# Performance work log

Measured on AMD Instinct MI355X. Metric: run time of the kernel, lower is better.

## Reference

```python
import jax, jax.numpy as jnp
import numpy as np

N, E, C = 100000, 50000, 256
M, D, F, T = 128, 128, 128, 64
MSG = 2 * D + F + T  # 448
T_MAX = 100000


def setup_inputs() -> dict:
    key = jax.random.key(0)
    ks = jax.random.split(key, 16)
    src = jax.random.randint(ks[0], (E,), 0, N, dtype=jnp.int32)
    dst = jax.random.randint(ks[1], (E,), 0, N, dtype=jnp.int32)
    t = jnp.sort(jax.random.randint(ks[2], (E,), 0, T_MAX, dtype=jnp.int32))
    last_update = jax.random.randint(ks[3], (N,), 0, 1000, dtype=jnp.int32)
    event_feat = jax.random.normal(ks[4], (E, F), dtype=jnp.float32)
    src_embeds = jax.random.normal(ks[5], (E, D), dtype=jnp.float32)
    dst_embeds = jax.random.normal(ks[6], (E, D), dtype=jnp.float32)
    nodes_memory = jax.random.normal(ks[7], (N, M), dtype=jnp.float32)
    incidence = jax.random.uniform(ks[8], (N, C), dtype=jnp.float32)
    w_time = jax.random.normal(ks[9], (T,), dtype=jnp.float32)
    b_time = jax.random.normal(ks[10], (T,), dtype=jnp.float32)
    W_ih = jax.random.normal(ks[11], (MSG, 3 * M), dtype=jnp.float32) * 0.05
    W_hh = jax.random.normal(ks[12], (M, 3 * M), dtype=jnp.float32) * 0.05
    b_ih = jnp.zeros((3 * M,), jnp.float32)
    b_hh = jnp.zeros((3 * M,), jnp.float32)
    return dict(src=src, dst=dst, t=t, last_update=last_update,
                event_feat=event_feat, src_embeds=src_embeds, dst_embeds=dst_embeds,
                nodes_memory=nodes_memory, incidence=incidence,
                w_time=w_time, b_time=b_time, W_ih=W_ih, W_hh=W_hh,
                b_ih=b_ih, b_hh=b_hh)


def reference(src, dst, t, last_update, event_feat, src_embeds, dst_embeds,
              nodes_memory, incidence, w_time, b_time, W_ih, W_hh, b_ih, b_hh):
    E2 = 2 * E
    # store_events: raw messages + flipped-direction messages, keyed by source node
    src_all = jnp.concatenate([src, dst])            # [2E]
    emb_s = jnp.concatenate([src_embeds, dst_embeds], axis=0)
    emb_d = jnp.concatenate([dst_embeds, src_embeds], axis=0)
    feat = jnp.concatenate([event_feat, event_feat], axis=0)
    t_all = jnp.concatenate([t, t])                  # [2E]
    # message function: concat(src_embed, dst_embed, event_feat, time_encoding(dt))
    dt = (t_all - last_update[src_all]).astype(jnp.float32)
    time_enc = jnp.cos(dt[:, None] * w_time[None, :] + b_time[None, :])  # [2E, T]
    msg = jnp.concatenate([emb_s, emb_d, feat, time_enc], axis=-1)       # [2E, MSG]
    # 'last' aggregation: per-node argmax over timestamps via rank-encoded segment_max
    perm = jnp.argsort(t_all)  # ascending time order
    rank = jnp.zeros((E2,), jnp.int32).at[perm].set(jnp.arange(E2, dtype=jnp.int32))
    seg_rank = jax.ops.segment_max(rank, src_all, num_segments=N)
    counts = jax.ops.segment_sum(jnp.ones((E2,), jnp.int32), src_all, num_segments=N)
    has_msg = counts > 0                              # [N]
    last_idx = perm[jnp.where(has_msg, seg_rank, 0)]  # [N] event index of last message
    agg_msg = msg[last_idx]                           # [N, MSG]
    # GRU memory updater (torch.nn.GRUCell convention)
    gx = agg_msg @ W_ih + b_ih
    gh = nodes_memory @ W_hh + b_hh
    xr, xz, xn = jnp.split(gx, 3, axis=-1)
    hr, hz, hn = jnp.split(gh, 3, axis=-1)
    r = jax.nn.sigmoid(xr + hr)
    z = jax.nn.sigmoid(xz + hz)
    n = jnp.tanh(xn + r * hn)
    h_new = (1.0 - z) * n + z * nodes_memory
    new_mem = jnp.where(has_msg[:, None], h_new, nodes_memory)  # [N, M]
    # rewire_graph: community memory = incidence.T @ nodes_memory
    comm_mem = jnp.einsum('nc,nm->cm', incidence, new_mem)      # [C, M]
    return jnp.concatenate([new_mem, comm_mem], axis=0)         # [N + C, M]
```

## Files before the change

kernel.cpp:

```cpp
#include <hip/hip_runtime.h>
#include <hip/hip_bf16.h>
#include <stdint.h>

#define N_NODES   100000
#define N_EVENTS  50000
#define N_COMM    256
#define DIM_M     128
#define K_TOT     576
#define GCOLS     512
#define INV2PI    0.15915494309189535f

typedef float f32x4 __attribute__((ext_vector_type(4)));
typedef short s16x8 __attribute__((ext_vector_type(8)));
typedef short s16x4 __attribute__((ext_vector_type(4)));

#define KEYS_OFF   0
#define CNT_OFF    800000
#define LIST_OFF   800008
#define W2PI_OFF   1200128
#define B2PI_OFF   1200384
#define WT_OFF     1200640
#define X_ROWS     100096
#define X_OFF      1790464
#define PART_M_OFF X_OFF
#define CT_NCH     256
#define CT_CPN     392
#define TMP2_OFF   (PART_M_OFF + 33554432)
#define TENC_OFF   1790464
#define PART_F_OFF 14594560

__device__ inline unsigned short f2bf(float x) {
    union { float f; unsigned u; } v; v.f = x;
    unsigned r = v.u + 0x7FFFu + ((v.u >> 16) & 1u);
    return (unsigned short)(r >> 16);
}
__device__ inline float bf2f(unsigned short u) {
    union { unsigned u; float f; } v; v.u = ((unsigned)u) << 16;
    return v.f;
}
__device__ inline float cos_rev(float rev) {
    float fr = rev - floorf(rev);
#if __has_builtin(__builtin_amdgcn_cosf)
    return __builtin_amdgcn_cosf(fr);
#else
    return cosf(fr * 6.283185307179586f);
#endif
}
__device__ inline float sigmoid_f(float x) { return 1.0f / (1.0f + __expf(-x)); }
__device__ inline float tanh_f(float x) {
    float t = __expf(2.0f * x);
    return 1.0f - 2.0f / (t + 1.0f);
}

__global__ __launch_bounds__(256) void k_agg(const int* __restrict__ src,
                                             const int* __restrict__ dst,
                                             const int* __restrict__ t,
                                             unsigned long long* __restrict__ keys) {
    int i = blockIdx.x * 256 + threadIdx.x;
    if (i >= 2 * N_EVENTS) return;
    int e = (i < N_EVENTS) ? i : i - N_EVENTS;
    int node = (i < N_EVENTS) ? src[i] : dst[e];
    unsigned long long key =
        ((unsigned long long)(unsigned)t[e] << 32) | (unsigned)(i + 1);
    atomicMax(&keys[node], key);
}

__global__ __launch_bounds__(256) void k_compact(const unsigned long long* __restrict__ keys,
                                                 unsigned int* __restrict__ cnt,
                                                 int* __restrict__ list) {
    int n = blockIdx.x * 256 + threadIdx.x;
    if (n >= N_NODES) return;
    if (keys[n] != 0ULL) {
        unsigned p = atomicAdd(cnt, 1u);
        list[p] = n;
    }
}

__global__ void k_prep(const float* __restrict__ w_time, const float* __restrict__ b_time,
                       float* __restrict__ w2, float* __restrict__ b2) {
    int i = threadIdx.x;
    if (i < 64) { w2[i] = w_time[i] * INV2PI; b2[i] = b_time[i] * INV2PI; }
}

__global__ __launch_bounds__(256) void k_wconv(const float* __restrict__ W_ih,
                                               const float* __restrict__ W_hh,
                                               unsigned short* __restrict__ Wt) {
    int idx = blockIdx.x * 256 + threadIdx.x;
    if (idx >= GCOLS * K_TOT) return;
    int col2 = idx / K_TOT, k = idx % K_TOT;
    int mh = col2 >> 8, rem = col2 & 255;
    int g = rem >> 6, m = mh * 64 + (rem & 63);
    float v;
    if (g == 0)      v = (k < 448) ? W_ih[(size_t)k * 384 + m]
                                   : W_hh[(size_t)(k - 448) * 384 + m];
    else if (g == 1) v = (k < 448) ? W_ih[(size_t)k * 384 + 128 + m]
                                   : W_hh[(size_t)(k - 448) * 384 + 128 + m];
    else if (g == 2) v = (k < 448) ? W_ih[(size_t)k * 384 + 256 + m] : 0.0f;
    else             v = (k < 448) ? 0.0f : W_hh[(size_t)(k - 448) * 384 + 256 + m];
    Wt[idx] = f2bf(v);
}

__global__ __launch_bounds__(256) void k_wconv_old(const float* __restrict__ W_ih,
                                                   const float* __restrict__ W_hh,
                                                   unsigned short* __restrict__ Wt) {
    int idx = blockIdx.x * 256 + threadIdx.x;
    if (idx >= GCOLS * K_TOT) return;
    int col = idx / K_TOT, k = idx % K_TOT;
    float v;
    if (col < 256) {
        v = (k < 448) ? W_ih[(size_t)k * 384 + col]
                      : W_hh[(size_t)(k - 448) * 384 + col];
    } else if (col < 384) {
        v = (k < 448) ? W_ih[(size_t)k * 384 + col] : 0.0f;
    } else {
        v = (k < 448) ? 0.0f : W_hh[(size_t)(k - 448) * 384 + (col - 128)];
    }
    Wt[idx] = f2bf(v);
}

__global__ __launch_bounds__(256) void k_xbuild(
    const unsigned long long* __restrict__ keys,
    const unsigned int* __restrict__ cnt,
    const int* __restrict__ list,
    const int* __restrict__ t,
    const int* __restrict__ last_update,
    const float* __restrict__ event_feat,
    const float* __restrict__ src_embeds,
    const float* __restrict__ dst_embeds,
    const float* __restrict__ mem,
    const float* __restrict__ w2pi,
    const float* __restrict__ b2pi,
    unsigned short* __restrict__ X) {
    const unsigned c = *cnt;
    const unsigned cpad = (c + 127u) & ~127u;
    const unsigned total = cpad * 72u;
    for (unsigned idx = blockIdx.x * 256 + threadIdx.x; idx < total;
         idx += gridDim.x * 256) {
        const unsigned row = idx / 72u;
        const int s = (int)(idx - row * 72u);
        unsigned short* xp = X + (size_t)row * K_TOT + s * 8;
        s16x8 v;
        if (row >= c) {
#pragma unroll
            for (int j = 0; j < 8; ++j) v[j] = 0;
            *(s16x8*)xp = v;
            continue;
        }
        const int node = list[row];
        const unsigned long long key = keys[node];
        const int ia = (int)(key & 0xffffffffull) - 1;
        const int e = (ia < N_EVENTS) ? ia : ia - N_EVENTS;
        if (s < 48) {
            const float* p;
            if (s < 16)
                p = ((ia < N_EVENTS) ? src_embeds : dst_embeds) + (size_t)e * 128 + s * 8;
            else if (s < 32)
                p = ((ia < N_EVENTS) ? dst_embeds : src_embeds) + (size_t)e * 128 + (s - 16) * 8;
            else
                p = event_feat + (size_t)e * 128 + (s - 32) * 8;
            float4 a = *(const float4*)p;
            float4 b = *(const float4*)(p + 4);
            v[0] = (short)f2bf(a.x); v[1] = (short)f2bf(a.y);
            v[2] = (short)f2bf(a.z); v[3] = (short)f2bf(a.w);
            v[4] = (short)f2bf(b.x); v[5] = (short)f2bf(b.y);
            v[6] = (short)f2bf(b.z); v[7] = (short)f2bf(b.w);
        } else if (s < 56) {
            const float dt = (float)(t[e] - last_update[node]);
            const int c0 = (s - 48) * 8;
#pragma unroll
            for (int j = 0; j < 8; ++j) {
                float rev = fmaf(dt, w2pi[c0 + j], b2pi[c0 + j]);
                v[j] = (short)f2bf(cos_rev(rev));
            }
        } else {
            const float* p = mem + (size_t)node * 128 + (s - 56) * 8;
            float4 a = *(const float4*)p;
            float4 b = *(const float4*)(p + 4);
            v[0] = (short)f2bf(a.x); v[1] = (short)f2bf(a.y);
            v[2] = (short)f2bf(a.z); v[3] = (short)f2bf(a.w);
            v[4] = (short)f2bf(b.x); v[5] = (short)f2bf(b.y);
            v[6] = (short)f2bf(b.z); v[7] = (short)f2bf(b.w);
        }
        *(s16x8*)xp = v;
    }
}

__global__ __launch_bounds__(512, 4) void k_gemm2(
    const unsigned int* __restrict__ cnt,
    const int* __restrict__ list,
    const unsigned short* __restrict__ X,
    const unsigned short* __restrict__ Wt,
    const float* __restrict__ b_ih,
    const float* __restrict__ b_hh,
    float* __restrict__ out) {
    __shared__ unsigned short As[3][128][64];
    __shared__ unsigned short Bs[3][256][64];
    __shared__ int Ls[128];

    const unsigned c = *cnt;
    const int rb = blockIdx.x >> 1;
    const int mh = blockIdx.x & 1;
    const int base = rb * 128;
    if ((unsigned)base >= c) return;
    const int tid = threadIdx.x;
    const int w = tid >> 6, l = tid & 63;
    const int lr = l & 15, lk = l >> 4;
    const int wm = w >> 2, wn = w & 3;

    if (tid < 128)
        Ls[tid] = ((unsigned)(base + tid) < c) ? list[base + tid] : 0;

    const int r8 = tid >> 3;
    const int sj = tid & 7;
    const int srcsl = (sj ^ (r8 & 7)) << 3;
    const unsigned short* gA0 = X + (size_t)(base + r8) * K_TOT + srcsl;
    const unsigned short* gA1 = X + (size_t)(base + 64 + r8) * K_TOT + srcsl;
    const unsigned short* gB0 = Wt + (size_t)(mh * 256 + r8) * K_TOT + srcsl;

#define GLD(SRC, DST) __builtin_amdgcn_global_load_lds( \
        (const __attribute__((address_space(1))) unsigned int*)(SRC), \
        (__attribute__((address_space(3))) unsigned int*)(DST), 16, 0, 0)

    auto stage = [&](int ch, int buf) {
        GLD(gA0 + ch * 64, &As[buf][w * 8][0]);
        GLD(gA1 + ch * 64, &As[buf][64 + w * 8][0]);
        GLD(gB0 + ch * 64,                          &Bs[buf][w * 8][0]);
        GLD(gB0 + (size_t)64 * K_TOT + ch * 64,     &Bs[buf][64 + w * 8][0]);
        GLD(gB0 + (size_t)128 * K_TOT + ch * 64,    &Bs[buf][128 + w * 8][0]);
        GLD(gB0 + (size_t)192 * K_TOT + ch * 64,    &Bs[buf][192 + w * 8][0]);
    };

    f32x4 acc[4][4];
#pragma unroll
    for (int rt = 0; rt < 4; ++rt)
#pragma unroll
        for (int i = 0; i < 4; ++i) acc[rt][i] = (f32x4){0.f, 0.f, 0.f, 0.f};

    stage(0, 0);
    stage(1, 1);
    __syncthreads();

#pragma unroll
    for (int ch = 0; ch < 9; ++ch) {
        const int buf = ch % 3;
        if (ch <= 6) stage(ch + 2, (ch + 2) % 3);
        __builtin_amdgcn_s_setprio(1);
#pragma unroll
        for (int ks = 0; ks < 2; ++ks) {
            s16x8 a[4];
#pragma unroll
            for (int rt = 0; rt < 4; ++rt) {
                const int r = wm * 64 + rt * 16 + lr;
                const int sl = (ks * 4 + lk) ^ (r & 7);
                a[rt] = *(const s16x8*)&As[buf][r][sl << 3];
            }
#pragma unroll
            for (int i = 0; i < 4; ++i) {
                const int col = i * 64 + wn * 16 + lr;
                const int slb = (ks * 4 + lk) ^ (col & 7);
                s16x8 b = *(const s16x8*)&Bs[buf][col][slb << 3];
#pragma unroll
                for (int rt = 0; rt < 4; ++rt)
                    acc[rt][i] = __builtin_amdgcn_mfma_f32_16x16x32_bf16(
                        a[rt], b, acc[rt][i], 0, 0, 0);
            }
        }
        __builtin_amdgcn_s_setprio(0);
        if (ch < 8) {
            __builtin_amdgcn_sched_barrier(0);
            if (ch < 7) asm volatile("s_waitcnt vmcnt(6)" ::: "memory");
            else        asm volatile("s_waitcnt vmcnt(0)" ::: "memory");
            __builtin_amdgcn_s_barrier();
            __builtin_amdgcn_sched_barrier(0);
        }
    }

    const int mcol = mh * 64 + wn * 16 + lr;
    const float b_r  = b_ih[mcol] + b_hh[mcol];
    const float b_z  = b_ih[128 + mcol] + b_hh[128 + mcol];
    const float b_xn = b_ih[256 + mcol];
    const float b_hn = b_hh[256 + mcol];
    const int hbuf = (mcol < 64) ? 1 : 2;
    const int kk   = (mcol < 64) ? mcol : mcol - 64;
#pragma unroll
    for (int rt = 0; rt < 4; ++rt) {
#pragma unroll
        for (int reg = 0; reg < 4; ++reg) {
            const int r = wm * 64 + rt * 16 + lk * 4 + reg;
            const int grow = base + r;
            if ((unsigned)grow < c) {
                const int node = Ls[r];
                const float h = bf2f(As[hbuf][r][(((kk >> 3) ^ (r & 7)) << 3) + (kk & 7)]);
                float rr = sigmoid_f(acc[rt][0][reg] + b_r);
                float zz = sigmoid_f(acc[rt][1][reg] + b_z);
                float nn = tanh_f(acc[rt][2][reg] + b_xn + rr * (acc[rt][3][reg] + b_hn));
                out[(size_t)node * 128 + mcol] = (1.0f - zz) * nn + zz * h;
            }
        }
    }
#undef GLD
}

__global__ __launch_bounds__(256) void k_copy(const unsigned long long* __restrict__ keys,
                                              const float* __restrict__ nm,
                                              float* __restrict__ out) {
    int idx = blockIdx.x * 256 + threadIdx.x;
    int n = idx >> 5;
    if (n >= N_NODES) return;
    if (keys[n] != 0ULL) return;
    ((float4*)out)[idx] = ((const float4*)nm)[idx];
}

__global__ __launch_bounds__(512) void k_comm_t(const float* __restrict__ inc,
                                                const float* __restrict__ nm,
                                                float* __restrict__ partials) {
    __shared__ unsigned short T[2][12288];

    const int bid = blockIdx.x;
    const int n0 = bid * CT_CPN;
    const int n1 = min(N_NODES, n0 + CT_CPN);
    const int ng = (n1 - n0 + 31) >> 5;
    const int tid = threadIdx.x;
    const int w = tid >> 6, l = tid & 63;
    const int lr = l & 15, lk = l >> 4;

    float vi[4][4];
    float vm[4][2];

    auto load_chunk = [&](int g) {
        const int nb = n0 + g * 32 + w * 4;
#pragma unroll
        for (int ri = 0; ri < 4; ++ri) {
            const int n = nb + ri;
            const bool ok = n < n1;
#pragma unroll
            for (int j = 0; j < 4; ++j)
                vi[ri][j] = ok ? inc[(size_t)n * N_COMM + l + 64 * j] : 0.0f;
#pragma unroll
            for (int j = 0; j < 2; ++j)
                vm[ri][j] = ok ? nm[(size_t)n * DIM_M + l + 64 * j] : 0.0f;
        }
    };
    auto write_chunk = [&](int buf) {
        unsigned short* bi = &T[buf][0];
#pragma unroll
        for (int j = 0; j < 4; ++j) {
            const int cc = l + 64 * j;
            ushort4 p = make_ushort4(f2bf(vi[0][j]), f2bf(vi[1][j]),
                                     f2bf(vi[2][j]), f2bf(vi[3][j]));
            *(ushort4*)&bi[cc * 32 + ((w ^ (cc & 7)) << 2)] = p;
        }
        unsigned short* bm = &T[buf][8192];
#pragma unroll
        for (int j = 0; j < 2; ++j) {
            const int mm = l + 64 * j;
            ushort4 p = make_ushort4(f2bf(vm[0][j]), f2bf(vm[1][j]),
                                     f2bf(vm[2][j]), f2bf(vm[3][j]));
            *(ushort4*)&bm[mm * 32 + ((w ^ (mm & 7)) << 2)] = p;
        }
    };

    f32x4 acc[2][8];
#pragma unroll
    for (int ct = 0; ct < 2; ++ct)
#pragma unroll
        for (int mt = 0; mt < 8; ++mt) acc[ct][mt] = (f32x4){0.f, 0.f, 0.f, 0.f};

    auto compute_chunk = [&](int buf) {
        const unsigned short* bi = &T[buf][0];
        const unsigned short* bm = &T[buf][8192];
        s16x8 a[2];
#pragma unroll
        for (int ct = 0; ct < 2; ++ct) {
            const int cc = (w * 2 + ct) * 16 + lr;
            s16x4 lo = *(const s16x4*)&bi[cc * 32 + (((lk * 2) ^ (cc & 7)) << 2)];
            s16x4 hi = *(const s16x4*)&bi[cc * 32 + (((lk * 2 + 1) ^ (cc & 7)) << 2)];
            a[ct] = __builtin_shufflevector(lo, hi, 0, 1, 2, 3, 4, 5, 6, 7);
        }
#pragma unroll
        for (int mt = 0; mt < 8; ++mt) {
            const int mm = mt * 16 + lr;
            s16x4 lo = *(const s16x4*)&bm[mm * 32 + (((lk * 2) ^ (mm & 7)) << 2)];
            s16x4 hi = *(const s16x4*)&bm[mm * 32 + (((lk * 2 + 1) ^ (mm & 7)) << 2)];
            s16x8 b = __builtin_shufflevector(lo, hi, 0, 1, 2, 3, 4, 5, 6, 7);
            acc[0][mt] = __builtin_amdgcn_mfma_f32_16x16x32_bf16(a[0], b, acc[0][mt], 0, 0, 0);
            acc[1][mt] = __builtin_amdgcn_mfma_f32_16x16x32_bf16(a[1], b, acc[1][mt], 0, 0, 0);
        }
    };

    load_chunk(0);
    write_chunk(0);
    __syncthreads();
    for (int g = 0; g < ng; ++g) {
        if (g + 1 < ng) load_chunk(g + 1);
        compute_chunk(g & 1);
        if (g + 1 < ng) write_chunk((g + 1) & 1);
        __syncthreads();
    }

    float* p = partials + (size_t)bid * (N_COMM * DIM_M);
#pragma unroll
    for (int ct = 0; ct < 2; ++ct) {
#pragma unroll
        for (int mt = 0; mt < 8; ++mt) {
#pragma unroll
            for (int reg = 0; reg < 4; ++reg) {
                const int cc = (w * 2 + ct) * 16 + lk * 4 + reg;
                p[(size_t)cc * DIM_M + mt * 16 + lr] = acc[ct][mt][reg];
            }
        }
    }
}

__global__ __launch_bounds__(256) void k_comm2a(const float* __restrict__ partials,
                                                float* __restrict__ tmp) {
    const int bid = blockIdx.x;
    const int y = bid >> 5, x = bid & 31;
    const int idx4 = x * 256 + threadIdx.x;
    float4 s = make_float4(0.f, 0.f, 0.f, 0.f);
    for (int ci = 0; ci < CT_NCH / 16; ++ci) {
        float4 v = *(const float4*)&partials[(size_t)(y * (CT_NCH / 16) + ci) * (N_COMM * DIM_M) + idx4 * 4];
        s.x += v.x; s.y += v.y; s.z += v.z; s.w += v.w;
    }
    *(float4*)&tmp[(size_t)y * (N_COMM * DIM_M) + idx4 * 4] = s;
}

__global__ __launch_bounds__(256) void k_comm2b(const float* __restrict__ tmp,
                                                float* __restrict__ out) {
    const int idx4 = blockIdx.x * 256 + threadIdx.x;
    float4 s = make_float4(0.f, 0.f, 0.f, 0.f);
    for (int y = 0; y < 16; ++y) {
        float4 v = *(const float4*)&tmp[(size_t)y * (N_COMM * DIM_M) + idx4 * 4];
        s.x += v.x; s.y += v.y; s.z += v.z; s.w += v.w;
    }
    *(float4*)&out[(size_t)N_NODES * DIM_M + idx4 * 4] = s;
}

__global__ __launch_bounds__(256) void k_tenc(const unsigned long long* __restrict__ keys,
                                              const unsigned int* __restrict__ cnt,
                                              const int* __restrict__ list,
                                              const int* __restrict__ t,
                                              const int* __restrict__ last_update,
                                              const float* __restrict__ w_time,
                                              const float* __restrict__ b_time,
                                              unsigned short* __restrict__ tenc) {
    int idx = blockIdx.x * 256 + threadIdx.x;
    int r = idx >> 3, slot = idx & 7;
    const unsigned c = *cnt;
    const unsigned cpad = (c + 63u) & ~63u;
    if ((unsigned)r >= cpad) return;
    s16x8 v;
    if ((unsigned)r < c) {
        int node = list[r];
        unsigned long long key = keys[node];
        int ia = (int)(key & 0xffffffffull) - 1;
        int e = (ia < N_EVENTS) ? ia : ia - N_EVENTS;
        float dt = (float)(t[e] - last_update[node]);
#pragma unroll
        for (int j = 0; j < 8; ++j) {
            int cix = slot * 8 + j;
            float arg = __fadd_rn(__fmul_rn(dt, w_time[cix]), b_time[cix]);
            v[j] = (short)f2bf(cosf(arg));
        }
    } else {
#pragma unroll
        for (int j = 0; j < 8; ++j) v[j] = 0;
    }
    *(s16x8*)&tenc[(size_t)r * 64 + slot * 8] = v;
}

__global__ __launch_bounds__(256, 2) void k_gemm_fused(
    const unsigned long long* __restrict__ keys,
    const unsigned int* __restrict__ cnt,
    const int* __restrict__ list,
    const float* __restrict__ event_feat,
    const float* __restrict__ src_embeds,
    const float* __restrict__ dst_embeds,
    const float* __restrict__ mem,
    const unsigned short* __restrict__ tenc,
    const unsigned short* __restrict__ Wt,
    const float* __restrict__ b_ih,
    const float* __restrict__ b_hh,
    float* __restrict__ out) {
    __shared__ unsigned short Xs[2][4][64][8];

    const unsigned c = *cnt;
    const int base = blockIdx.x * 64;
    if ((unsigned)base >= c) return;
    const int tid = threadIdx.x;

    const int srow = tid >> 2;
    const int kslot = tid & 3;
    const int sgrow = base + srow;
    const bool valid = (unsigned)sgrow < c;
    const float *p_es = nullptr, *p_ed = nullptr, *p_ef = nullptr, *p_mem = nullptr;
    const unsigned short* p_te = nullptr;
    if (valid) {
        int node = list[sgrow];
        unsigned long long key = keys[node];
        int ia = (int)(key & 0xffffffffull) - 1;
        int e = (ia < N_EVENTS) ? ia : ia - N_EVENTS;
        const float* sp = src_embeds + (size_t)e * 128;
        const float* dp = dst_embeds + (size_t)e * 128;
        p_es = (ia < N_EVENTS) ? sp : dp;
        p_ed = (ia < N_EVENTS) ? dp : sp;
        p_ef = event_feat + (size_t)e * 128;
        p_te = tenc + (size_t)sgrow * 64;
        p_mem = mem + (size_t)node * 128;
    }

    auto stage = [&](int ch) {
        const int buf = ch & 1;
        const int k0 = ch * 32 + kslot * 8;
        s16x8 v;
        if (valid) {
            if (k0 < 384) {
                const float* p = (k0 < 128) ? (p_es + k0)
                               : (k0 < 256) ? (p_ed + (k0 - 128))
                                            : (p_ef + (k0 - 256));
                float4 a = *(const float4*)p;
                float4 b = *(const float4*)(p + 4);
                v[0] = (short)f2bf(a.x); v[1] = (short)f2bf(a.y);
                v[2] = (short)f2bf(a.z); v[3] = (short)f2bf(a.w);
                v[4] = (short)f2bf(b.x); v[5] = (short)f2bf(b.y);
                v[6] = (short)f2bf(b.z); v[7] = (short)f2bf(b.w);
            } else if (k0 < 448) {
                v = *(const s16x8*)(p_te + (k0 - 384));
            } else {
                const float* p = p_mem + (k0 - 448);
                float4 a = *(const float4*)p;
                float4 b = *(const float4*)(p + 4);
                v[0] = (short)f2bf(a.x); v[1] = (short)f2bf(a.y);
                v[2] = (short)f2bf(a.z); v[3] = (short)f2bf(a.w);
                v[4] = (short)f2bf(b.x); v[5] = (short)f2bf(b.y);
                v[6] = (short)f2bf(b.z); v[7] = (short)f2bf(b.w);
            }
        } else {
#pragma unroll
            for (int j = 0; j < 8; ++j) v[j] = 0;
        }
        *(s16x8*)&Xs[buf][kslot][srow][0] = v;
    };

    const int w = tid >> 6;
    const int l = tid & 63;
    const int lr = l & 15;
    const int lk = l >> 4;

    f32x4 acc[4][8];
#pragma unroll
    for (int rt = 0; rt < 4; ++rt)
#pragma unroll
        for (int i = 0; i < 8; ++i) acc[rt][i] = (f32x4){0.f, 0.f, 0.f, 0.f};

    stage(0);
    __syncthreads();

    for (int ch = 0; ch < 18; ++ch) {
        if (ch < 17) stage(ch + 1);
        const int buf = ch & 1;
        s16x8 a[4];
#pragma unroll
        for (int rt = 0; rt < 4; ++rt)
            a[rt] = *(const s16x8*)&Xs[buf][lk][rt * 16 + lr][0];
#pragma unroll
        for (int i = 0; i < 8; ++i) {
            const int col = (w + 4 * i) * 16 + lr;
            s16x8 b = *(const s16x8*)&Wt[(size_t)col * K_TOT + ch * 32 + lk * 8];
#pragma unroll
            for (int rt = 0; rt < 4; ++rt)
                acc[rt][i] = __builtin_amdgcn_mfma_f32_16x16x32_bf16(
                    a[rt], b, acc[rt][i], 0, 0, 0);
        }
        __syncthreads();
    }

#pragma unroll
    for (int jj = 0; jj < 2; ++jj) {
        const int mcol = (w + 4 * jj) * 16 + lr;
        const float b_r  = b_ih[mcol] + b_hh[mcol];
        const float b_z  = b_ih[128 + mcol] + b_hh[128 + mcol];
        const float b_xn = b_ih[256 + mcol];
        const float b_hn = b_hh[256 + mcol];
#pragma unroll
        for (int rt = 0; rt < 4; ++rt) {
#pragma unroll
            for (int reg = 0; reg < 4; ++reg) {
                const int grow = base + rt * 16 + lk * 4 + reg;
                if ((unsigned)grow < c) {
                    const int node = list[grow];
                    const float h = mem[(size_t)node * 128 + mcol];
                    float rr = sigmoid_f(acc[rt][0 + jj][reg] + b_r);
                    float zz = sigmoid_f(acc[rt][2 + jj][reg] + b_z);
                    float nn = tanh_f(acc[rt][4 + jj][reg] + b_xn +
                                      rr * (acc[rt][6 + jj][reg] + b_hn));
                    out[(size_t)node * 128 + mcol] = (1.0f - zz) * nn + zz * h;
                }
            }
        }
    }
}

__global__ __launch_bounds__(256) void k_comm1(const float* __restrict__ inc,
                                               const float* __restrict__ nm,
                                               float* __restrict__ partials,
                                               int nch, int cpn) {
    __shared__ float inc_s[2][8][128];
    __shared__ float mem_s[2][8][128];

    const int bid = blockIdx.x;
    const int ct2 = bid / nch;
    const int ch  = bid % nch;
    const int n0 = ch * cpn;
    const int n1 = min(N_NODES, n0 + cpn);
    const int tid = threadIdx.x;

    const int srow = tid >> 5;
    const int scol = (tid & 31) * 4;

    auto stage = [&](int g, int buf) {
        const int n = n0 + g * 8 + srow;
        float4 iv = make_float4(0.f, 0.f, 0.f, 0.f);
        float4 mv = make_float4(0.f, 0.f, 0.f, 0.f);
        if (n < n1) {
            iv = *(const float4*)(inc + (size_t)n * N_COMM + ct2 * 128 + scol);
            mv = *(const float4*)(nm + (size_t)n * DIM_M + scol);
        }
        *(float4*)&inc_s[buf][srow][scol] = iv;
        *(float4*)&mem_s[buf][srow][scol] = mv;
    };

    const int c0 = (tid >> 3) * 4;
    const int mb = (tid & 7) * 4;

    float acc[4][4][4];
#pragma unroll
    for (int a = 0; a < 4; ++a)
#pragma unroll
        for (int b = 0; b < 4; ++b)
#pragma unroll
            for (int d = 0; d < 4; ++d) acc[a][b][d] = 0.0f;

    const int ngrp = (n1 - n0 + 7) >> 3;
    stage(0, 0);
    __syncthreads();

    for (int g = 0; g < ngrp; ++g) {
        if (g + 1 < ngrp) stage(g + 1, (g + 1) & 1);
        const int buf = g & 1;
#pragma unroll
        for (int i = 0; i < 8; ++i) {
            const float4 cv = *(const float4*)&inc_s[buf][i][c0];
            const float ca[4] = {cv.x, cv.y, cv.z, cv.w};
#pragma unroll
            for (int j = 0; j < 4; ++j) {
                const float4 mv = *(const float4*)&mem_s[buf][i][j * 32 + mb];
                const float ma[4] = {mv.x, mv.y, mv.z, mv.w};
#pragma unroll
                for (int ci = 0; ci < 4; ++ci)
#pragma unroll
                    for (int mi = 0; mi < 4; ++mi)
                        acc[ci][j][mi] = fmaf(ca[ci], ma[mi], acc[ci][j][mi]);
            }
        }
        __syncthreads();
    }

    float* p = partials + (size_t)bid * (128 * 128);
#pragma unroll
    for (int ci = 0; ci < 4; ++ci)
#pragma unroll
        for (int j = 0; j < 4; ++j)
            *(float4*)(p + (size_t)(c0 + ci) * 128 + j * 32 + mb) =
                make_float4(acc[ci][j][0], acc[ci][j][1], acc[ci][j][2], acc[ci][j][3]);
}

__global__ __launch_bounds__(256) void k_comm2_f(const float* __restrict__ partials,
                                                 float* __restrict__ out,
                                                 int nch) {
    int idx = blockIdx.x * 256 + threadIdx.x;
    if (idx >= N_COMM * DIM_M) return;
    int cg = idx >> 7;
    int m = idx & 127;
    int ct2 = cg >> 7;
    int cl = cg & 127;
    float s = 0.0f;
    for (int ch = 0; ch < nch; ++ch)
        s += partials[((size_t)ct2 * nch + ch) * 16384 + (size_t)cl * 128 + m];
    out[(size_t)N_NODES * DIM_M + idx] = s;
}

extern "C" void kernel_launch(void* const* d_in, const int* in_sizes, int n_in,
                              void* d_out, int out_size, void* d_ws, size_t ws_size,
                              hipStream_t stream) {
    const int* src          = (const int*)d_in[0];
    const int* dst          = (const int*)d_in[1];
    const int* t            = (const int*)d_in[2];
    const int* last_update  = (const int*)d_in[3];
    const float* event_feat = (const float*)d_in[4];
    const float* src_embeds = (const float*)d_in[5];
    const float* dst_embeds = (const float*)d_in[6];
    const float* nodes_mem  = (const float*)d_in[7];
    const float* incidence  = (const float*)d_in[8];
    const float* w_time     = (const float*)d_in[9];
    const float* b_time     = (const float*)d_in[10];
    const float* W_ih       = (const float*)d_in[11];
    const float* W_hh       = (const float*)d_in[12];
    const float* b_ih       = (const float*)d_in[13];
    const float* b_hh       = (const float*)d_in[14];
    float* out = (float*)d_out;

    char* ws = (char*)d_ws;
    unsigned long long* keys = (unsigned long long*)(ws + KEYS_OFF);
    unsigned int* cnt        = (unsigned int*)(ws + CNT_OFF);
    int* list                = (int*)(ws + LIST_OFF);
    float* w2pi              = (float*)(ws + W2PI_OFF);
    float* b2pi              = (float*)(ws + B2PI_OFF);
    unsigned short* Wt       = (unsigned short*)(ws + WT_OFF);

    const bool xfit = ws_size >= (size_t)X_OFF + (size_t)X_ROWS * (K_TOT * 2);

    hipMemsetAsync(d_ws, 0, LIST_OFF, stream);

    k_agg<<<(2 * N_EVENTS + 255) / 256, 256, 0, stream>>>(src, dst, t, keys);
    k_compact<<<(N_NODES + 255) / 256, 256, 0, stream>>>(keys, cnt, list);
    k_prep<<<1, 64, 0, stream>>>(w_time, b_time, w2pi, b2pi);

    if (xfit) {
        unsigned short* X = (unsigned short*)(ws + X_OFF);
        float* partials   = (float*)(ws + PART_M_OFF);
        float* tmp2       = (float*)(ws + TMP2_OFF);

        k_wconv<<<(GCOLS * K_TOT + 255) / 256, 256, 0, stream>>>(W_ih, W_hh, Wt);
        k_xbuild<<<4096, 256, 0, stream>>>(keys, cnt, list, t, last_update,
                                           event_feat, src_embeds, dst_embeds,
                                           nodes_mem, w2pi, b2pi, X);
        k_gemm2<<<(X_ROWS / 128) * 2, 512, 0, stream>>>(cnt, list, X, Wt, b_ih, b_hh, out);
        k_copy<<<(N_NODES * 32 + 255) / 256, 256, 0, stream>>>(keys, nodes_mem, out);
        k_comm_t<<<CT_NCH, 512, 0, stream>>>(incidence, out, partials);
        k_comm2a<<<512, 256, 0, stream>>>(partials, tmp2);
        k_comm2b<<<32, 256, 0, stream>>>(tmp2, out);
    } else {
        unsigned short* tenc = (unsigned short*)(ws + TENC_OFF);
        float* partials      = (float*)(ws + PART_F_OFF);
        int NCH = 512;
        while (NCH > 8 && (size_t)PART_F_OFF + (size_t)NCH * 131072 > ws_size) NCH >>= 1;
        int cpn = (N_NODES + NCH - 1) / NCH;

        k_wconv_old<<<(GCOLS * K_TOT + 255) / 256, 256, 0, stream>>>(W_ih, W_hh, Wt);
        k_tenc<<<(100032 * 8) / 256, 256, 0, stream>>>(keys, cnt, list, t, last_update,
                                                       w_time, b_time, tenc);
        k_gemm_fused<<<100032 / 64, 256, 0, stream>>>(keys, cnt, list, event_feat,
                                                      src_embeds, dst_embeds, nodes_mem,
                                                      tenc, Wt, b_ih, b_hh, out);
        k_copy<<<(N_NODES * 32 + 255) / 256, 256, 0, stream>>>(keys, nodes_mem, out);
        k_comm1<<<2 * NCH, 256, 0, stream>>>(incidence, out, partials, NCH, cpn);
        k_comm2_f<<<(N_COMM * DIM_M + 255) / 256, 256, 0, stream>>>(partials, out, NCH);
    }
}
```

Measured before the change: 203.0 us.

## Fuse weight conversion and time-prep into xbuild; shrink GEMM K-tile to 32

Removes the k_prep and k_wconv launches by folding weight bf16 conversion into extra blocks of k_xbuild and computing the scaled time weights inline. The GEMM now stages K in 32-wide chunks (18 iterations) with a new swizzle, cutting LDS use per block. It loads the hidden-state values from global memory into registers up front instead of reading them from a retained LDS buffer. The aim is fewer launches and higher occupancy, at the cost of more barrier iterations and extra global loads.

Result: no change. 201.8 us (-0.6%).

```diff
diff --git a/kernel.cpp b/kernel.cpp
--- a/kernel.cpp
+++ b/kernel.cpp
@@ -9,6 +9,7 @@
 #define K_TOT     576
 #define GCOLS     512
 #define INV2PI    0.15915494309189535f
+#define XB_GRID   4096
 
 typedef float f32x4 __attribute__((ext_vector_type(4)));
 typedef short s16x8 __attribute__((ext_vector_type(8)));
@@ -17,8 +18,6 @@
 #define KEYS_OFF   0
 #define CNT_OFF    800000
 #define LIST_OFF   800008
-#define W2PI_OFF   1200128
-#define B2PI_OFF   1200384
 #define WT_OFF     1200640
 #define X_ROWS     100096
 #define X_OFF      1790464
@@ -76,48 +75,6 @@
     }
 }
 
-__global__ void k_prep(const float* __restrict__ w_time, const float* __restrict__ b_time,
-                       float* __restrict__ w2, float* __restrict__ b2) {
-    int i = threadIdx.x;
-    if (i < 64) { w2[i] = w_time[i] * INV2PI; b2[i] = b_time[i] * INV2PI; }
-}
-
-__global__ __launch_bounds__(256) void k_wconv(const float* __restrict__ W_ih,
-                                               const float* __restrict__ W_hh,
-                                               unsigned short* __restrict__ Wt) {
-    int idx = blockIdx.x * 256 + threadIdx.x;
-    if (idx >= GCOLS * K_TOT) return;
-    int col2 = idx / K_TOT, k = idx % K_TOT;
-    int mh = col2 >> 8, rem = col2 & 255;
-    int g = rem >> 6, m = mh * 64 + (rem & 63);
-    float v;
-    if (g == 0)      v = (k < 448) ? W_ih[(size_t)k * 384 + m]
-                                   : W_hh[(size_t)(k - 448) * 384 + m];
-    else if (g == 1) v = (k < 448) ? W_ih[(size_t)k * 384 + 128 + m]
-                                   : W_hh[(size_t)(k - 448) * 384 + 128 + m];
-    else if (g == 2) v = (k < 448) ? W_ih[(size_t)k * 384 + 256 + m] : 0.0f;
-    else             v = (k < 448) ? 0.0f : W_hh[(size_t)(k - 448) * 384 + 256 + m];
-    Wt[idx] = f2bf(v);
-}
-
-__global__ __launch_bounds__(256) void k_wconv_old(const float* __restrict__ W_ih,
-                                                   const float* __restrict__ W_hh,
-                                                   unsigned short* __restrict__ Wt) {
-    int idx = blockIdx.x * 256 + threadIdx.x;
-    if (idx >= GCOLS * K_TOT) return;
-    int col = idx / K_TOT, k = idx % K_TOT;
-    float v;
-    if (col < 256) {
-        v = (k < 448) ? W_ih[(size_t)k * 384 + col]
-                      : W_hh[(size_t)(k - 448) * 384 + col];
-    } else if (col < 384) {
-        v = (k < 448) ? W_ih[(size_t)k * 384 + col] : 0.0f;
-    } else {
-        v = (k < 448) ? 0.0f : W_hh[(size_t)(k - 448) * 384 + (col - 128)];
-    }
-    Wt[idx] = f2bf(v);
-}
-
 __global__ __launch_bounds__(256) void k_xbuild(
     const unsigned long long* __restrict__ keys,
     const unsigned int* __restrict__ cnt,
@@ -128,14 +85,33 @@
     const float* __restrict__ src_embeds,
     const float* __restrict__ dst_embeds,
     const float* __restrict__ mem,
-    const float* __restrict__ w2pi,
-    const float* __restrict__ b2pi,
+    const float* __restrict__ w_time,
+    const float* __restrict__ b_time,
+    const float* __restrict__ W_ih,
+    const float* __restrict__ W_hh,
+    unsigned short* __restrict__ Wt,
     unsigned short* __restrict__ X) {
+    if (blockIdx.x >= XB_GRID) {
+        int idx = (blockIdx.x - XB_GRID) * 256 + threadIdx.x;
+        if (idx >= GCOLS * K_TOT) return;
+        int col2 = idx / K_TOT, k = idx % K_TOT;
+        int mh = col2 >> 8, rem = col2 & 255;
+        int g = rem >> 6, m = mh * 64 + (rem & 63);
+        float v;
+        if (g == 0)      v = (k < 448) ? W_ih[(size_t)k * 384 + m]
+                                       : W_hh[(size_t)(k - 448) * 384 + m];
+        else if (g == 1) v = (k < 448) ? W_ih[(size_t)k * 384 + 128 + m]
+                                       : W_hh[(size_t)(k - 448) * 384 + 128 + m];
+        else if (g == 2) v = (k < 448) ? W_ih[(size_t)k * 384 + 256 + m] : 0.0f;
+        else             v = (k < 448) ? 0.0f : W_hh[(size_t)(k - 448) * 384 + 256 + m];
+        Wt[idx] = f2bf(v);
+        return;
+    }
     const unsigned c = *cnt;
     const unsigned cpad = (c + 127u) & ~127u;
     const unsigned total = cpad * 72u;
     for (unsigned idx = blockIdx.x * 256 + threadIdx.x; idx < total;
-         idx += gridDim.x * 256) {
+         idx += XB_GRID * 256) {
         const unsigned row = idx / 72u;
         const int s = (int)(idx - row * 72u);
         unsigned short* xp = X + (size_t)row * K_TOT + s * 8;
@@ -169,7 +145,7 @@
             const int c0 = (s - 48) * 8;
 #pragma unroll
             for (int j = 0; j < 8; ++j) {
-                float rev = fmaf(dt, w2pi[c0 + j], b2pi[c0 + j]);
+                float rev = fmaf(dt, w_time[c0 + j] * INV2PI, b_time[c0 + j] * INV2PI);
                 v[j] = (short)f2bf(cos_rev(rev));
             }
         } else {
@@ -193,8 +169,8 @@
     const float* __restrict__ b_ih,
     const float* __restrict__ b_hh,
     float* __restrict__ out) {
-    __shared__ unsigned short As[3][128][64];
-    __shared__ unsigned short Bs[3][256][64];
+    __shared__ unsigned short As[3][128][32];
+    __shared__ unsigned short Bs[3][256][32];
     __shared__ int Ls[128];
 
     const unsigned c = *cnt;
@@ -210,24 +186,32 @@
     if (tid < 128)
         Ls[tid] = ((unsigned)(base + tid) < c) ? list[base + tid] : 0;
 
-    const int r8 = tid >> 3;
-    const int sj = tid & 7;
-    const int srcsl = (sj ^ (r8 & 7)) << 3;
-    const unsigned short* gA0 = X + (size_t)(base + r8) * K_TOT + srcsl;
-    const unsigned short* gA1 = X + (size_t)(base + 64 + r8) * K_TOT + srcsl;
-    const unsigned short* gB0 = Wt + (size_t)(mh * 256 + r8) * K_TOT + srcsl;
+    const int mcol = mh * 64 + wn * 16 + lr;
+
+    unsigned short hreg[16];
+#pragma unroll
+    for (int rt = 0; rt < 4; ++rt)
+#pragma unroll
+        for (int reg = 0; reg < 4; ++reg) {
+            const int r = wm * 64 + rt * 16 + lk * 4 + reg;
+            hreg[rt * 4 + reg] = X[(size_t)(base + r) * K_TOT + 448 + mcol];
+        }
+
+    const int srow = tid >> 2;
+    const int sd = tid & 3;
+    const int ssl = (sd ^ ((srow >> 1) & 3)) << 3;
+    const unsigned short* gA  = X  + (size_t)(base + srow) * K_TOT + ssl;
+    const unsigned short* gB0 = Wt + (size_t)(mh * 256 + srow) * K_TOT + ssl;
+    const unsigned short* gB1 = Wt + (size_t)(mh * 256 + 128 + srow) * K_TOT + ssl;
 
 #define GLD(SRC, DST) __builtin_amdgcn_global_load_lds( \
         (const __attribute__((address_space(1))) unsigned int*)(SRC), \
         (__attribute__((address_space(3))) unsigned int*)(DST), 16, 0, 0)
 
     auto stage = [&](int ch, int buf) {
-        GLD(gA0 + ch * 64, &As[buf][w * 8][0]);
-        GLD(gA1 + ch * 64, &As[buf][64 + w * 8][0]);
-        GLD(gB0 + ch * 64,                          &Bs[buf][w * 8][0]);
-        GLD(gB0 + (size_t)64 * K_TOT + ch * 64,     &Bs[buf][64 + w * 8][0]);
-        GLD(gB0 + (size_t)128 * K_TOT + ch * 64,    &Bs[buf][128 + w * 8][0]);
-        GLD(gB0 + (size_t)192 * K_TOT + ch * 64,    &Bs[buf][192 + w * 8][0]);
+        GLD(gA  + ch * 32, &As[buf][w * 16][0]);
+        GLD(gB0 + ch * 32, &Bs[buf][w * 16][0]);
+        GLD(gB1 + ch * 32, &Bs[buf][128 + w * 16][0]);
     };
 
     f32x4 acc[4][4];
@@ -241,47 +225,41 @@
     __syncthreads();
 
 #pragma unroll
-    for (int ch = 0; ch < 9; ++ch) {
+    for (int ch = 0; ch < 18; ++ch) {
         const int buf = ch % 3;
-        if (ch <= 6) stage(ch + 2, (ch + 2) % 3);
+        if (ch <= 15) stage(ch + 2, (ch + 2) % 3);
         __builtin_amdgcn_s_setprio(1);
-#pragma unroll
-        for (int ks = 0; ks < 2; ++ks) {
-            s16x8 a[4];
-#pragma unroll
-            for (int rt = 0; rt < 4; ++rt) {
-                const int r = wm * 64 + rt * 16 + lr;
-                const int sl = (ks * 4 + lk) ^ (r & 7);
-                a[rt] = *(const s16x8*)&As[buf][r][sl << 3];
-            }
-#pragma unroll
-            for (int i = 0; i < 4; ++i) {
-                const int col = i * 64 + wn * 16 + lr;
-                const int slb = (ks * 4 + lk) ^ (col & 7);
-                s16x8 b = *(const s16x8*)&Bs[buf][col][slb << 3];
-#pragma unroll
-                for (int rt = 0; rt < 4; ++rt)
-                    acc[rt][i] = __builtin_amdgcn_mfma_f32_16x16x32_bf16(
-                        a[rt], b, acc[rt][i], 0, 0, 0);
-            }
+        s16x8 a[4];
+#pragma unroll
+        for (int rt = 0; rt < 4; ++rt) {
+            const int r = wm * 64 + rt * 16 + lr;
+            const int sl = lk ^ ((r >> 1) & 3);
+            a[rt] = *(const s16x8*)&As[buf][r][sl << 3];
+        }
+#pragma unroll
+        for (int i = 0; i < 4; ++i) {
+            const int cl = i * 64 + wn * 16 + lr;
+            const int slb = lk ^ ((cl >> 1) & 3);
+            s16x8 b = *(const s16x8*)&Bs[buf][cl][slb << 3];
+#pragma unroll
+            for (int rt = 0; rt < 4; ++rt)
+                acc[rt][i] = __builtin_amdgcn_mfma_f32_16x16x32_bf16(
+                    a[rt], b, acc[rt][i], 0, 0, 0);
         }
         __builtin_amdgcn_s_setprio(0);
-        if (ch < 8) {
+        if (ch < 17) {
             __builtin_amdgcn_sched_barrier(0);
-            if (ch < 7) asm volatile("s_waitcnt vmcnt(6)" ::: "memory");
-            else        asm volatile("s_waitcnt vmcnt(0)" ::: "memory");
+            if (ch < 16) asm volatile("s_waitcnt vmcnt(3)" ::: "memory");
+            else         asm volatile("s_waitcnt vmcnt(0)" ::: "memory");
             __builtin_amdgcn_s_barrier();
             __builtin_amdgcn_sched_barrier(0);
         }
     }
 
-    const int mcol = mh * 64 + wn * 16 + lr;
     const float b_r  = b_ih[mcol] + b_hh[mcol];
     const float b_z  = b_ih[128 + mcol] + b_hh[128 + mcol];
     const float b_xn = b_ih[256 + mcol];
     const float b_hn = b_hh[256 + mcol];
-    const int hbuf = (mcol < 64) ? 1 : 2;
-    const int kk   = (mcol < 64) ? mcol : mcol - 64;
 #pragma unroll
     for (int rt = 0; rt < 4; ++rt) {
 #pragma unroll
@@ -290,7 +268,7 @@
             const int grow = base + r;
             if ((unsigned)grow < c) {
                 const int node = Ls[r];
-                const float h = bf2f(As[hbuf][r][(((kk >> 3) ^ (r & 7)) << 3) + (kk & 7)]);
+                const float h = bf2f(hreg[rt * 4 + reg]);
                 float rr = sigmoid_f(acc[rt][0][reg] + b_r);
                 float zz = sigmoid_f(acc[rt][1][reg] + b_z);
                 float nn = tanh_f(acc[rt][2][reg] + b_xn + rr * (acc[rt][3][reg] + b_hn));
@@ -434,6 +412,24 @@
         s.x += v.x; s.y += v.y; s.z += v.z; s.w += v.w;
     }
     *(float4*)&out[(size_t)N_NODES * DIM_M + idx4 * 4] = s;
+}
+
+__global__ __launch_bounds__(256) void k_wconv_old(const float* __restrict__ W_ih,
+                                                   const float* __restrict__ W_hh,
+                                                   unsigned short* __restrict__ Wt) {
+    int idx = blockIdx.x * 256 + threadIdx.x;
+    if (idx >= GCOLS * K_TOT) return;
+    int col = idx / K_TOT, k = idx % K_TOT;
+    float v;
+    if (col < 256) {
+        v = (k < 448) ? W_ih[(size_t)k * 384 + col]
+                      : W_hh[(size_t)(k - 448) * 384 + col];
+    } else if (col < 384) {
+        v = (k < 448) ? W_ih[(size_t)k * 384 + col] : 0.0f;
+    } else {
+        v = (k < 448) ? 0.0f : W_hh[(size_t)(k - 448) * 384 + (col - 128)];
+    }
+    Wt[idx] = f2bf(v);
 }
 
 __global__ __launch_bounds__(256) void k_tenc(const unsigned long long* __restrict__ keys,
@@ -714,8 +710,6 @@
     unsigned long long* keys = (unsigned long long*)(ws + KEYS_OFF);
     unsigned int* cnt        = (unsigned int*)(ws + CNT_OFF);
     int* list                = (int*)(ws + LIST_OFF);
-    float* w2pi              = (float*)(ws + W2PI_OFF);
-    float* b2pi              = (float*)(ws + B2PI_OFF);
     unsigned short* Wt       = (unsigned short*)(ws + WT_OFF);
 
     const bool xfit = ws_size >= (size_t)X_OFF + (size_t)X_ROWS * (K_TOT * 2);
@@ -724,17 +718,16 @@
 
     k_agg<<<(2 * N_EVENTS + 255) / 256, 256, 0, stream>>>(src, dst, t, keys);
     k_compact<<<(N_NODES + 255) / 256, 256, 0, stream>>>(keys, cnt, list);
-    k_prep<<<1, 64, 0, stream>>>(w_time, b_time, w2pi, b2pi);
 
     if (xfit) {
         unsigned short* X = (unsigned short*)(ws + X_OFF);
         float* partials   = (float*)(ws + PART_M_OFF);
         float* tmp2       = (float*)(ws + TMP2_OFF);
 
-        k_wconv<<<(GCOLS * K_TOT + 255) / 256, 256, 0, stream>>>(W_ih, W_hh, Wt);
-        k_xbuild<<<4096, 256, 0, stream>>>(keys, cnt, list, t, last_update,
-                                           event_feat, src_embeds, dst_embeds,
-                                           nodes_mem, w2pi, b2pi, X);
+        const int wconv_blocks = (GCOLS * K_TOT + 255) / 256;
+        k_xbuild<<<XB_GRID + wconv_blocks, 256, 0, stream>>>(
+            keys, cnt, list, t, last_update, event_feat, src_embeds, dst_embeds,
+            nodes_mem, w_time, b_time, W_ih, W_hh, Wt, X);
         k_gemm2<<<(X_ROWS / 128) * 2, 512, 0, stream>>>(cnt, list, X, Wt, b_ih, b_hh, out);
         k_copy<<<(N_NODES * 32 + 255) / 256, 256, 0, stream>>>(keys, nodes_mem, out);
         k_comm_t<<<CT_NCH, 512, 0, stream>>>(incidence, out, partials);
```
